# Kernel tuning notes

Measured on AMD Instinct MI355X. Metric: run time of the kernel, lower is better.

## Reference

```python
import jax, jax.numpy as jnp
import numpy as np

N_NODES = 100000
N_EDGES = 1500000
N_REL = 3
HID = 256


def setup_inputs() -> dict:
    key = jax.random.key(0)
    ks = jax.random.split(key, 8)
    return {
        "feat_a": jax.random.normal(ks[0], (N_NODES, 256), dtype=jnp.float32),
        "feat_b": jax.random.normal(ks[1], (N_NODES, 384), dtype=jnp.float32),
        "Wp_a": jax.random.normal(ks[2], (256, HID), dtype=jnp.float32) * 0.03,
        "Wp_b": jax.random.normal(ks[3], (384, HID), dtype=jnp.float32) * 0.03,
        "Wr": jax.random.normal(ks[4], (N_REL, HID, HID), dtype=jnp.float32) * 0.06,
        "ln_gamma": jnp.ones((HID,), dtype=jnp.float32),
        "ln_beta": jnp.zeros((HID,), dtype=jnp.float32),
        "edge_weight": jax.random.uniform(ks[5], (N_EDGES,), dtype=jnp.float32),
        "edge_src": jax.random.randint(ks[6], (N_EDGES,), 0, N_NODES, dtype=jnp.int32),
        "edge_dst": jax.random.randint(ks[7], (N_EDGES,), 0, N_NODES, dtype=jnp.int32),
    }


def _layer_norm(x, gamma, beta, eps=1e-5):
    mu = jnp.mean(x, axis=-1, keepdims=True)
    var = jnp.mean(jnp.square(x - mu), axis=-1, keepdims=True)
    return (x - mu) * jax.lax.rsqrt(var + eps) * gamma + beta


def reference(feat_a, feat_b, Wp_a, Wp_b, Wr, ln_gamma, ln_beta,
              edge_weight, edge_src, edge_dst):
    # avg fusion of modality projections (bias-free linears), padding node zeroed
    h0 = 0.5 * (feat_a @ Wp_a + feat_b @ Wp_b)  # [N, H]
    h0 = h0.at[0].set(0.0)

    n = h0.shape[0]
    e_per_rel = edge_src.shape[0] // N_REL  # edges pre-sorted by relation id
    aggregated = jnp.zeros_like(h0)
    for r in range(N_REL):
        s = slice(r * e_per_rel, (r + 1) * e_per_rel)
        src, dst, w = edge_src[s], edge_dst[s], edge_weight[s]
        # gather -> relation linear -> weight scale  [E_r, H]
        msg = (h0[src] @ Wr[r]) * w[:, None]
        num = jax.ops.segment_sum(msg, dst, num_segments=n)
        den = jax.ops.segment_sum(w, dst, num_segments=n)
        aggregated = aggregated + num / jnp.maximum(den, 1e-8)[:, None]

    # dropout p=0 / eval -> identity; residual + LayerNorm, padding node zeroed
    h1 = _layer_norm(h0 + aggregated, ln_gamma, ln_beta)
    h1 = h1.at[0].set(0.0)
    return h1
```

## Files before the change

### kernel.cpp

```cpp
#include <hip/hip_runtime.h>

#define N_NODES 100000
#define HID 256
#define N_EDGES 1500000
#define N_REL 3
#define E_PER_REL (N_EDGES / N_REL)
#define NKEYS (N_REL * N_NODES)
#define KP 640
#define KR 768

#define SCAN_CHUNK 1024
#define NSCANBLK ((NKEYS + SCAN_CHUNK - 1) / SCAN_CHUNK)

typedef __attribute__((ext_vector_type(8))) short bf16x8;
typedef __attribute__((ext_vector_type(4))) float f32x4;

__device__ __forceinline__ short f2bf(float x) {
    union { float f; unsigned u; } v; v.f = x;
    unsigned r = v.u + 0x7fffu + ((v.u >> 16) & 1u);
    return (short)(r >> 16);
}
__device__ __forceinline__ float bf2f(short h) {
    union { unsigned u; float f; } v;
    v.u = ((unsigned)(unsigned short)h) << 16;
    return v.f;
}
__device__ __forceinline__ int xorf(int r) { return (r & 3) ^ ((r >> 2) & 3); }

__device__ __forceinline__ void gload16(const void* g, void* l) {
    typedef const __attribute__((address_space(1))) unsigned int gq;
    typedef __attribute__((address_space(3))) unsigned int lq;
    __builtin_amdgcn_global_load_lds((gq*)g, (lq*)l, 16, 0, 0);
}

__global__ __launch_bounds__(256) void wprep_kernel(
    const float* __restrict__ Wa, const float* __restrict__ Wb,
    const float* __restrict__ Wr,
    short* __restrict__ WTp, short* __restrict__ WTr)
{
    int idx = blockIdx.x * 256 + threadIdx.x;
    if (idx < 256 * KP) {
        int c = idx / KP, k = idx - c * KP;
        float v = (k < 256) ? Wa[k * HID + c] : Wb[(k - 256) * HID + c];
        WTp[idx] = f2bf(0.5f * v);
    } else {
        int j = idx - 256 * KP;
        if (j < 256 * KR) {
            int c = j / KR, k = j - c * KR;
            WTr[j] = f2bf(Wr[(k >> 8) * HID * HID + (k & 255) * HID + c]);
        }
    }
}

__global__ __launch_bounds__(512, 4) void proj_gemm(
    const float* __restrict__ fa, const float* __restrict__ fb,
    const short* __restrict__ WTp, short* __restrict__ h0h)
{
    __shared__ float smA[2][128 * 32];
    __shared__ short smB[2][256 * 32];
    const int tid = threadIdx.x;
    const int lane = tid & 63;
    const int w = tid >> 6;
    const int wr = w >> 2, wc = w & 3;
    const int brow = blockIdx.x * 128;

    f32x4 acc[4][4] = {};

    const int a_r8 = lane >> 3;
    const int a_sl = (lane & 7) ^ a_r8;
    const int b_c16 = lane >> 2;

    int aRowG[2], bColL[2], bSl[2];
    #pragma unroll
    for (int ii = 0; ii < 2; ++ii) {
        int i = w * 2 + ii;
        int gr = brow + i * 8 + a_r8;
        aRowG[ii] = (gr < N_NODES) ? gr : (N_NODES - 1);
        bColL[ii] = i * 16 + b_c16;
        bSl[ii] = (lane & 3) ^ xorf(bColL[ii]);
    }

    auto stage = [&](int buf, int k0) {
        const float* asrc; int astr, kk;
        if (k0 < 256) { asrc = fa; astr = 256; kk = k0; }
        else          { asrc = fb; astr = 384; kk = k0 - 256; }
        #pragma unroll
        for (int ii = 0; ii < 2; ++ii) {
            int i = w * 2 + ii;
            gload16(asrc + (size_t)aRowG[ii] * astr + kk + a_sl * 4,
                    (char*)&smA[buf][0] + i * 1024);
        }
        #pragma unroll
        for (int ii = 0; ii < 2; ++ii) {
            int i = w * 2 + ii;
            gload16(WTp + (size_t)bColL[ii] * KP + k0 + bSl[ii] * 8,
                    (char*)&smB[buf][0] + i * 1024);
        }
    };

    stage(0, 0);
    __syncthreads();
    int cur = 0;
    for (int t = 0; t < KP / 32; ++t) {
        int knext = (t + 1) * 32;
        if (knext < KP) stage(cur ^ 1, knext);

        bf16x8 afr[4], bfr[4];
        #pragma unroll
        for (int m = 0; m < 4; ++m) {
            int rt = wr * 64 + m * 16 + (lane & 15);
            int p0 = (((lane >> 4) << 1) | 0) ^ (rt & 7);
            int p1 = (((lane >> 4) << 1) | 1) ^ (rt & 7);
            f32x4 lo = *(const f32x4*)((const char*)&smA[cur][0] + rt * 128 + p0 * 16);
            f32x4 hi = *(const f32x4*)((const char*)&smA[cur][0] + rt * 128 + p1 * 16);
            bf16x8 tb;
            tb[0] = f2bf(lo.x); tb[1] = f2bf(lo.y); tb[2] = f2bf(lo.z); tb[3] = f2bf(lo.w);
            tb[4] = f2bf(hi.x); tb[5] = f2bf(hi.y); tb[6] = f2bf(hi.z); tb[7] = f2bf(hi.w);
            afr[m] = tb;
        }
        #pragma unroll
        for (int n = 0; n < 4; ++n) {
            int ct = wc * 64 + n * 16 + (lane & 15);
            int p = (lane >> 4) ^ xorf(ct);
            bfr[n] = *(const bf16x8*)((const char*)&smB[cur][0] + ct * 64 + p * 16);
        }
        #pragma unroll
        for (int m = 0; m < 4; ++m)
            #pragma unroll
            for (int n = 0; n < 4; ++n)
                acc[m][n] = __builtin_amdgcn_mfma_f32_16x16x32_bf16(
                    afr[m], bfr[n], acc[m][n], 0, 0, 0);

        __syncthreads();
        cur ^= 1;
    }

    #pragma unroll
    for (int m = 0; m < 4; ++m) {
        #pragma unroll
        for (int j = 0; j < 4; ++j) {
            int row = brow + wr * 64 + m * 16 + ((lane >> 4) << 2) + j;
            if (row >= N_NODES) continue;
            #pragma unroll
            for (int n = 0; n < 4; ++n) {
                int col = wc * 64 + n * 16 + (lane & 15);
                short v = (row == 0) ? (short)0 : f2bf(acc[m][n][j]);
                h0h[(size_t)row * HID + col] = v;
            }
        }
    }
}

__global__ __launch_bounds__(512, 4) void rel_gemm_ln(
    const short* __restrict__ S, const short* __restrict__ WTr,
    const short* __restrict__ h0h,
    const float* __restrict__ gamma, const float* __restrict__ beta,
    float* __restrict__ out)
{
    __shared__ short smA[2][128 * 32];
    __shared__ short smB[2][256 * 32];
    __shared__ float redS[128][4];
    __shared__ float redS2[128][4];
    __shared__ float smMean[128], smRs[128];
    __shared__ float smG[256], smBt[256];
    const int tid = threadIdx.x;
    const int lane = tid & 63;
    const int w = tid >> 6;
    const int wr = w >> 2, wc = w & 3;
    const int brow = blockIdx.x * 128;

    if (tid < 256) { smG[tid] = gamma[tid]; smBt[tid] = beta[tid]; }

    f32x4 acc[4][4] = {};

    const int s_r16 = lane >> 2;
    const int sRowL = w * 16 + s_r16;
    int gr0 = brow + sRowL;
    const int sRowG = (gr0 < N_NODES) ? gr0 : (N_NODES - 1);
    const int sSl = (lane & 3) ^ xorf(sRowL);
    const int b_c16 = lane >> 2;
    int bColL[2], bSl[2];
    #pragma unroll
    for (int ii = 0; ii < 2; ++ii) {
        int i = w * 2 + ii;
        bColL[ii] = i * 16 + b_c16;
        bSl[ii] = (lane & 3) ^ xorf(bColL[ii]);
    }

    auto stage = [&](int buf, int k0) {
        gload16(S + (size_t)sRowG * KR + k0 + sSl * 8,
                (char*)&smA[buf][0] + w * 1024);
        #pragma unroll
        for (int ii = 0; ii < 2; ++ii) {
            int i = w * 2 + ii;
            gload16(WTr + (size_t)bColL[ii] * KR + k0 + bSl[ii] * 8,
                    (char*)&smB[buf][0] + i * 1024);
        }
    };

    stage(0, 0);
    __syncthreads();
    int cur = 0;
    for (int t = 0; t < KR / 32; ++t) {
        int knext = (t + 1) * 32;
        if (knext < KR) stage(cur ^ 1, knext);

        bf16x8 afr[4], bfr[4];
        #pragma unroll
        for (int m = 0; m < 4; ++m) {
            int rt = wr * 64 + m * 16 + (lane & 15);
            int p = (lane >> 4) ^ xorf(rt);
            afr[m] = *(const bf16x8*)((const char*)&smA[cur][0] + rt * 64 + p * 16);
        }
        #pragma unroll
        for (int n = 0; n < 4; ++n) {
            int ct = wc * 64 + n * 16 + (lane & 15);
            int p = (lane >> 4) ^ xorf(ct);
            bfr[n] = *(const bf16x8*)((const char*)&smB[cur][0] + ct * 64 + p * 16);
        }
        #pragma unroll
        for (int m = 0; m < 4; ++m)
            #pragma unroll
            for (int n = 0; n < 4; ++n)
                acc[m][n] = __builtin_amdgcn_mfma_f32_16x16x32_bf16(
                    afr[m], bfr[n], acc[m][n], 0, 0, 0);

        __syncthreads();
        cur ^= 1;
    }

    #pragma unroll
    for (int m = 0; m < 4; ++m) {
        #pragma unroll
        for (int j = 0; j < 4; ++j) {
            int lrow = wr * 64 + m * 16 + ((lane >> 4) << 2) + j;
            int grow = brow + lrow;
            int crow = (grow < N_NODES) ? grow : 0;
            float s = 0.f, s2 = 0.f;
            #pragma unroll
            for (int n = 0; n < 4; ++n) {
                int col = wc * 64 + n * 16 + (lane & 15);
                float x = acc[m][n][j] + bf2f(h0h[(size_t)crow * HID + col]);
                acc[m][n][j] = x;
                s += x; s2 = fmaf(x, x, s2);
            }
            #pragma unroll
            for (int off = 1; off < 16; off <<= 1) {
                s += __shfl_xor(s, off, 64);
                s2 += __shfl_xor(s2, off, 64);
            }
            if ((lane & 15) == 0) { redS[lrow][wc] = s; redS2[lrow][wc] = s2; }
        }
    }
    __syncthreads();
    if (tid < 128) {
        float tot  = redS[tid][0] + redS[tid][1] + redS[tid][2] + redS[tid][3];
        float tot2 = redS2[tid][0] + redS2[tid][1] + redS2[tid][2] + redS2[tid][3];
        float mean = tot * (1.0f / HID);
        float var = tot2 * (1.0f / HID) - mean * mean;
        smMean[tid] = mean;
        smRs[tid] = rsqrtf(var + 1e-5f);
    }
    __syncthreads();
    #pragma unroll
    for (int m = 0; m < 4; ++m) {
        #pragma unroll
        for (int j = 0; j < 4; ++j) {
            int lrow = wr * 64 + m * 16 + ((lane >> 4) << 2) + j;
            int grow = brow + lrow;
            if (grow >= N_NODES) continue;
            float mean = smMean[lrow], rs = smRs[lrow];
            #pragma unroll
            for (int n = 0; n < 4; ++n) {
                int col = wc * 64 + n * 16 + (lane & 15);
                float y = (acc[m][n][j] - mean) * rs * smG[col] + smBt[col];
                out[(size_t)grow * HID + col] = (grow == 0) ? 0.f : y;
            }
        }
    }
}

__global__ __launch_bounds__(256) void hist_kernel(
    const int* __restrict__ dst, int* __restrict__ count)
{
    int i = blockIdx.x * 256 + threadIdx.x;
    if (i >= N_EDGES) return;
    int r = i / E_PER_REL;
    atomicAdd(&count[r * N_NODES + dst[i]], 1);
}

__global__ __launch_bounds__(256) void scan1_kernel(
    const int* __restrict__ count, int* __restrict__ offset,
    int* __restrict__ bsum)
{
    __shared__ int tmp[256];
    const int t = threadIdx.x;
    const int base = blockIdx.x * SCAN_CHUNK + t * 4;
    int v[4];
    #pragma unroll
    for (int j = 0; j < 4; ++j)
        v[j] = (base + j < NKEYS) ? count[base + j] : 0;
    int tsum = v[0] + v[1] + v[2] + v[3];
    tmp[t] = tsum;
    __syncthreads();
    #pragma unroll
    for (int off = 1; off < 256; off <<= 1) {
        int x = (t >= off) ? tmp[t - off] : 0;
        __syncthreads();
        tmp[t] += x;
        __syncthreads();
    }
    int run = tmp[t] - tsum;
    #pragma unroll
    for (int j = 0; j < 4; ++j) {
        if (base + j < NKEYS) offset[base + j] = run;
        run += v[j];
    }
    if (t == 0) bsum[blockIdx.x] = tmp[255];
}

__global__ __launch_bounds__(256) void scan2_kernel(int* __restrict__ bsum)
{
    __shared__ int tmp[256];
    const int t = threadIdx.x;
    int v0 = (2 * t     < NSCANBLK) ? bsum[2 * t]     : 0;
    int v1 = (2 * t + 1 < NSCANBLK) ? bsum[2 * t + 1] : 0;
    int psum = v0 + v1;
    tmp[t] = psum;
    __syncthreads();
    #pragma unroll
    for (int off = 1; off < 256; off <<= 1) {
        int x = (t >= off) ? tmp[t - off] : 0;
        __syncthreads();
        tmp[t] += x;
        __syncthreads();
    }
    int excl = tmp[t] - psum;
    if (2 * t     < NSCANBLK) bsum[2 * t]     = excl;
    if (2 * t + 1 < NSCANBLK) bsum[2 * t + 1] = excl + v0;
}

__global__ __launch_bounds__(256) void scan3_kernel(
    int* __restrict__ offset, const int* __restrict__ bsum)
{
    int i = blockIdx.x * 256 + threadIdx.x;
    if (i >= NKEYS) return;
    offset[i] += bsum[i / SCAN_CHUNK];
}

__global__ __launch_bounds__(256) void fill_kernel(
    const int* __restrict__ src, const int* __restrict__ dst,
    const float* __restrict__ w,
    int* __restrict__ offset, int* __restrict__ csr_src,
    float* __restrict__ csr_w)
{
    int i = blockIdx.x * 256 + threadIdx.x;
    if (i >= N_EDGES) return;
    int r = i / E_PER_REL;
    int key = r * N_NODES + dst[i];
    int pos = atomicAdd(&offset[key], 1);
    csr_src[pos] = src[i];
    csr_w[pos] = w[i];
}

__global__ __launch_bounds__(256) void gather_kernel(
    const short* __restrict__ h0h,
    const int* __restrict__ ends, const int* __restrict__ count,
    const int* __restrict__ csr_src, const float* __restrict__ csr_w,
    short* __restrict__ S)
{
    int gw = (blockIdx.x * 256 + threadIdx.x) >> 6;
    int lane = threadIdx.x & 63;
    if (gw >= N_REL * N_NODES) return;
    int r = gw / N_NODES;
    int node = gw - r * N_NODES;
    int deg = count[gw];
    int end = ends[gw];
    int start = end - deg;
    const size_t colo = (size_t)lane * 4;

    float a0 = 0.f, a1 = 0.f, a2 = 0.f, a3 = 0.f;
    float den = 0.f;

    if (deg > 0) {
        int degc = (deg < 64) ? deg : 64;
        int myp = start + ((lane < degc) ? lane : 0);
        int msrc = csr_src[myp];
        float mw = (lane < degc) ? csr_w[myp] : 0.f;

        for (int p = 0; p < degc; p += 4) {
            #pragma unroll
            for (int j = 0; j < 4; ++j) {
                int q = p + j;
                bool ok = q < degc;
                int sj = __shfl(msrc, ok ? q : 0, 64);
                float wj = ok ? __shfl(mw, q, 64) : 0.f;
                short4 v = *(const short4*)(h0h + (size_t)sj * HID + colo);
                a0 = fmaf(wj, bf2f(v.x), a0);
                a1 = fmaf(wj, bf2f(v.y), a1);
                a2 = fmaf(wj, bf2f(v.z), a2);
                a3 = fmaf(wj, bf2f(v.w), a3);
                den += wj;
            }
        }
        for (int p = start + 64; p < end; ++p) {
            int s = csr_src[p];
            float wt = csr_w[p];
            short4 v = *(const short4*)(h0h + (size_t)s * HID + colo);
            a0 = fmaf(wt, bf2f(v.x), a0);
            a1 = fmaf(wt, bf2f(v.y), a1);
            a2 = fmaf(wt, bf2f(v.z), a2);
            a3 = fmaf(wt, bf2f(v.w), a3);
            den += wt;
        }
    }

    float inv = 1.0f / fmaxf(den, 1e-8f);
    short4 o;
    o.x = f2bf(a0 * inv);
    o.y = f2bf(a1 * inv);
    o.z = f2bf(a2 * inv);
    o.w = f2bf(a3 * inv);
    *(short4*)(S + (size_t)node * KR + r * HID + colo) = o;
}

extern "C" void kernel_launch(void* const* d_in, const int* in_sizes, int n_in,
                              void* d_out, int out_size, void* d_ws, size_t ws_size,
                              hipStream_t stream) {
    const float* fa    = (const float*)d_in[0];
    const float* fb    = (const float*)d_in[1];
    const float* Wa    = (const float*)d_in[2];
    const float* Wb    = (const float*)d_in[3];
    const float* Wr    = (const float*)d_in[4];
    const float* gamma = (const float*)d_in[5];
    const float* beta  = (const float*)d_in[6];
    const float* ew    = (const float*)d_in[7];
    const int*   esrc  = (const int*)d_in[8];
    const int*   edst  = (const int*)d_in[9];
    float* out = (float*)d_out;

    char* ws = (char*)d_ws;
    size_t off = 0;
    short* h0h     = (short*)(ws + off); off += (size_t)N_NODES * HID * 2;
    short* S       = (short*)(ws + off); off += (size_t)N_NODES * KR * 2;
    short* WTp     = (short*)(ws + off); off += (size_t)256 * KP * 2;
    short* WTr     = (short*)(ws + off); off += (size_t)256 * KR * 2;
    int*   count   = (int*)  (ws + off); off += (size_t)NKEYS * 4;
    int*   offs    = (int*)  (ws + off); off += (size_t)NKEYS * 4;
    int*   bsum    = (int*)  (ws + off); off += 4096;
    int*   csr_src = (int*)  (ws + off); off += (size_t)N_EDGES * 4;
    float* csr_w   = (float*)(ws + off); off += (size_t)N_EDGES * 4;

    wprep_kernel<<<(256 * KP + 256 * KR) / 256, 256, 0, stream>>>(
        Wa, Wb, Wr, WTp, WTr);

    const int ngrid = (N_NODES + 127) / 128;
    proj_gemm<<<ngrid, 512, 0, stream>>>(fa, fb, WTp, h0h);

    hipMemsetAsync(count, 0, (size_t)NKEYS * 4, stream);
    const int egrid = (N_EDGES + 255) / 256;
    hist_kernel<<<egrid, 256, 0, stream>>>(edst, count);
    scan1_kernel<<<NSCANBLK, 256, 0, stream>>>(count, offs, bsum);
    scan2_kernel<<<1, 256, 0, stream>>>(bsum);
    scan3_kernel<<<(NKEYS + 255) / 256, 256, 0, stream>>>(offs, bsum);
    fill_kernel<<<egrid, 256, 0, stream>>>(esrc, edst, ew, offs, csr_src, csr_w);

    gather_kernel<<<(N_REL * N_NODES * 64) / 256, 256, 0, stream>>>(
        h0h, offs, count, csr_src, csr_w, S);

    rel_gemm_ln<<<ngrid, 512, 0, stream>>>(S, WTr, h0h, gamma, beta, out);
}
```

Measured before the change: 527.7 us.

## Convert A tile to bf16 in registers before LDS and shrink shared memory

```diff
diff --git a/kernel.cpp b/kernel.cpp
--- a/kernel.cpp
+++ b/kernel.cpp
@@ -52,77 +52,71 @@
     }
 }
 
-__global__ __launch_bounds__(512, 4) void proj_gemm(
+__global__ __launch_bounds__(512, 8) void proj_gemm(
     const float* __restrict__ fa, const float* __restrict__ fb,
     const short* __restrict__ WTp, short* __restrict__ h0h)
 {
-    __shared__ float smA[2][128 * 32];
-    __shared__ short smB[2][256 * 32];
+    __shared__ alignas(16) char lds[49152];
     const int tid = threadIdx.x;
     const int lane = tid & 63;
     const int w = tid >> 6;
     const int wr = w >> 2, wc = w & 3;
     const int brow = blockIdx.x * 128;
 
+    auto smA = [&](int b) -> char* { return lds + b * 8192; };
+    auto smB = [&](int b) -> char* { return lds + 16384 + b * 16384; };
+
     f32x4 acc[4][4] = {};
 
-    const int a_r8 = lane >> 3;
-    const int a_sl = (lane & 7) ^ a_r8;
+    const int arow = tid >> 2;
+    const int akq = tid & 3;
+    int gr = brow + arow;
+    const int garow = (gr < N_NODES) ? gr : (N_NODES - 1);
+    const int aslot = akq ^ xorf(arow);
     const int b_c16 = lane >> 2;
-
-    int aRowG[2], bColL[2], bSl[2];
+    int bColL[2], bSl[2];
     #pragma unroll
     for (int ii = 0; ii < 2; ++ii) {
         int i = w * 2 + ii;
-        int gr = brow + i * 8 + a_r8;
-        aRowG[ii] = (gr < N_NODES) ? gr : (N_NODES - 1);
         bColL[ii] = i * 16 + b_c16;
         bSl[ii] = (lane & 3) ^ xorf(bColL[ii]);
     }
 
-    auto stage = [&](int buf, int k0) {
+    auto loadA = [&](int k0, f32x4& o0, f32x4& o1) {
         const float* asrc; int astr, kk;
         if (k0 < 256) { asrc = fa; astr = 256; kk = k0; }
         else          { asrc = fb; astr = 384; kk = k0 - 256; }
-        #pragma unroll
-        for (int ii = 0; ii < 2; ++ii) {
-            int i = w * 2 + ii;
-            gload16(asrc + (size_t)aRowG[ii] * astr + kk + a_sl * 4,
-                    (char*)&smA[buf][0] + i * 1024);
-        }
+        const float* ap = asrc + (size_t)garow * astr + kk + akq * 8;
+        o0 = *(const f32x4*)(ap + 0);
+        o1 = *(const f32x4*)(ap + 4);
+    };
+    auto writeA = [&](int buf, const f32x4& v0, const f32x4& v1) {
+        bf16x8 ha;
+        ha[0] = f2bf(v0.x); ha[1] = f2bf(v0.y); ha[2] = f2bf(v0.z); ha[3] = f2bf(v0.w);
+        ha[4] = f2bf(v1.x); ha[5] = f2bf(v1.y); ha[6] = f2bf(v1.z); ha[7] = f2bf(v1.w);
+        *(bf16x8*)(smA(buf) + arow * 64 + aslot * 16) = ha;
+    };
+    auto stageB = [&](int buf, int k0) {
         #pragma unroll
         for (int ii = 0; ii < 2; ++ii) {
             int i = w * 2 + ii;
             gload16(WTp + (size_t)bColL[ii] * KP + k0 + bSl[ii] * 8,
-                    (char*)&smB[buf][0] + i * 1024);
+                    smB(buf) + i * 1024);
         }
     };
-
-    stage(0, 0);
-    __syncthreads();
-    int cur = 0;
-    for (int t = 0; t < KP / 32; ++t) {
-        int knext = (t + 1) * 32;
-        if (knext < KP) stage(cur ^ 1, knext);
-
+    auto compute = [&](int buf) {
         bf16x8 afr[4], bfr[4];
         #pragma unroll
         for (int m = 0; m < 4; ++m) {
             int rt = wr * 64 + m * 16 + (lane & 15);
-            int p0 = (((lane >> 4) << 1) | 0) ^ (rt & 7);
-            int p1 = (((lane >> 4) << 1) | 1) ^ (rt & 7);
-            f32x4 lo = *(const f32x4*)((const char*)&smA[cur][0] + rt * 128 + p0 * 16);
-            f32x4 hi = *(const f32x4*)((const char*)&smA[cur][0] + rt * 128 + p1 * 16);
-            bf16x8 tb;
-            tb[0] = f2bf(lo.x); tb[1] = f2bf(lo.y); tb[2] = f2bf(lo.z); tb[3] = f2bf(lo.w);
-            tb[4] = f2bf(hi.x); tb[5] = f2bf(hi.y); tb[6] = f2bf(hi.z); tb[7] = f2bf(hi.w);
-            afr[m] = tb;
+            int p = (lane >> 4) ^ xorf(rt);
+            afr[m] = *(const bf16x8*)(smA(buf) + rt * 64 + p * 16);
         }
         #pragma unroll
         for (int n = 0; n < 4; ++n) {
             int ct = wc * 64 + n * 16 + (lane & 15);
             int p = (lane >> 4) ^ xorf(ct);
-            bfr[n] = *(const bf16x8*)((const char*)&smB[cur][0] + ct * 64 + p * 16);
+            bfr[n] = *(const bf16x8*)(smB(buf) + ct * 64 + p * 16);
         }
         #pragma unroll
         for (int m = 0; m < 4; ++m)
@@ -130,9 +124,29 @@
             for (int n = 0; n < 4; ++n)
                 acc[m][n] = __builtin_amdgcn_mfma_f32_16x16x32_bf16(
                     afr[m], bfr[n], acc[m][n], 0, 0, 0);
-
-        __syncthreads();
-        cur ^= 1;
+    };
+
+    const int nt = KP / 32;
+    f32x4 p0, p1, q0, q1;
+    loadA(0, p0, p1);
+    stageB(0, 0);
+    loadA(32, q0, q1);
+    writeA(0, p0, p1);
+    __syncthreads();
+
+    for (int t = 0; t < nt; t += 2) {
+        writeA(1, q0, q1);
+        stageB(1, (t + 1) * 32);
+        if (t + 2 < nt) loadA((t + 2) * 32, p0, p1);
+        compute(0);
+        __syncthreads();
+        if (t + 2 < nt) {
+            writeA(0, p0, p1);
+            stageB(0, (t + 2) * 32);
+            if (t + 3 < nt) loadA((t + 3) * 32, q0, q1);
+        }
+        compute(1);
+        __syncthreads();
     }
 
     #pragma unroll
@@ -151,25 +165,21 @@
     }
 }
 
-__global__ __launch_bounds__(512, 4) void rel_gemm_ln(
+__global__ __launch_bounds__(512, 8) void rel_gemm_ln(
     const short* __restrict__ S, const short* __restrict__ WTr,
     const short* __restrict__ h0h,
     const float* __restrict__ gamma, const float* __restrict__ beta,
     float* __restrict__ out)
 {
-    __shared__ short smA[2][128 * 32];
-    __shared__ short smB[2][256 * 32];
-    __shared__ float redS[128][4];
-    __shared__ float redS2[128][4];
-    __shared__ float smMean[128], smRs[128];
-    __shared__ float smG[256], smBt[256];
+    __shared__ alignas(16) char lds[49152];
     const int tid = threadIdx.x;
     const int lane = tid & 63;
     const int w = tid >> 6;
     const int wr = w >> 2, wc = w & 3;
     const int brow = blockIdx.x * 128;
 
-    if (tid < 256) { smG[tid] = gamma[tid]; smBt[tid] = beta[tid]; }
+    auto smA = [&](int b) -> char* { return lds + b * 8192; };
+    auto smB = [&](int b) -> char* { return lds + 16384 + b * 16384; };
 
     f32x4 acc[4][4] = {};
 
@@ -188,13 +198,12 @@
     }
 
     auto stage = [&](int buf, int k0) {
-        gload16(S + (size_t)sRowG * KR + k0 + sSl * 8,
-                (char*)&smA[buf][0] + w * 1024);
+        gload16(S + (size_t)sRowG * KR + k0 + sSl * 8, smA(buf) + w * 1024);
         #pragma unroll
         for (int ii = 0; ii < 2; ++ii) {
             int i = w * 2 + ii;
             gload16(WTr + (size_t)bColL[ii] * KR + k0 + bSl[ii] * 8,
-                    (char*)&smB[buf][0] + i * 1024);
+                    smB(buf) + i * 1024);
         }
     };
 
@@ -210,13 +219,13 @@
         for (int m = 0; m < 4; ++m) {
             int rt = wr * 64 + m * 16 + (lane & 15);
             int p = (lane >> 4) ^ xorf(rt);
-            afr[m] = *(const bf16x8*)((const char*)&smA[cur][0] + rt * 64 + p * 16);
+            afr[m] = *(const bf16x8*)(smA(cur) + rt * 64 + p * 16);
         }
         #pragma unroll
         for (int n = 0; n < 4; ++n) {
             int ct = wc * 64 + n * 16 + (lane & 15);
             int p = (lane >> 4) ^ xorf(ct);
-            bfr[n] = *(const bf16x8*)((const char*)&smB[cur][0] + ct * 64 + p * 16);
+            bfr[n] = *(const bf16x8*)(smB(cur) + ct * 64 + p * 16);
         }
         #pragma unroll
         for (int m = 0; m < 4; ++m)
@@ -227,6 +236,19 @@
 
         __syncthreads();
         cur ^= 1;
+    }
+
+    float* redS  = (float*)lds;
+    float* redS2 = redS + 512;
+    float* smMean = redS2 + 512;
+    float* smRs   = smMean + 128;
+
+    float gk[4], bk[4];
+    #pragma unroll
+    for (int n = 0; n < 4; ++n) {
+        int col = wc * 64 + n * 16 + (lane & 15);
+        gk[n] = gamma[col];
+        bk[n] = beta[col];
     }
 
     #pragma unroll
@@ -249,13 +271,13 @@
                 s += __shfl_xor(s, off, 64);
                 s2 += __shfl_xor(s2, off, 64);
             }
-            if ((lane & 15) == 0) { redS[lrow][wc] = s; redS2[lrow][wc] = s2; }
+            if ((lane & 15) == 0) { redS[lrow * 4 + wc] = s; redS2[lrow * 4 + wc] = s2; }
         }
     }
     __syncthreads();
     if (tid < 128) {
-        float tot  = redS[tid][0] + redS[tid][1] + redS[tid][2] + redS[tid][3];
-        float tot2 = redS2[tid][0] + redS2[tid][1] + redS2[tid][2] + redS2[tid][3];
+        float tot  = redS[tid * 4 + 0] + redS[tid * 4 + 1] + redS[tid * 4 + 2] + redS[tid * 4 + 3];
+        float tot2 = redS2[tid * 4 + 0] + redS2[tid * 4 + 1] + redS2[tid * 4 + 2] + redS2[tid * 4 + 3];
         float mean = tot * (1.0f / HID);
         float var = tot2 * (1.0f / HID) - mean * mean;
         smMean[tid] = mean;
@@ -273,7 +295,7 @@
             #pragma unroll
             for (int n = 0; n < 4; ++n) {
                 int col = wc * 64 + n * 16 + (lane & 15);
-                float y = (acc[m][n][j] - mean) * rs * smG[col] + smBt[col];
+                float y = (acc[m][n][j] - mean) * rs * gk[n] + bk[n];
                 out[(size_t)grow * HID + col] = (grow == 0) ? 0.f : y;
             }
         }
```

Measured after the change: 521.2 us. About the same (-1.2%).

## Triple-buffer LDS staging in both GEMMs with explicit vmcnt waits

Applied to the files above, without the earlier changes.

```diff
diff --git a/kernel.cpp b/kernel.cpp
--- a/kernel.cpp
+++ b/kernel.cpp
@@ -52,35 +52,41 @@
     }
 }
 
-__global__ __launch_bounds__(512, 4) void proj_gemm(
+__global__ __launch_bounds__(512, 2) void proj_gemm(
     const float* __restrict__ fa, const float* __restrict__ fb,
     const short* __restrict__ WTp, short* __restrict__ h0h)
 {
-    __shared__ float smA[2][128 * 32];
-    __shared__ short smB[2][256 * 32];
+    __shared__ alignas(16) char lds[98304];
     const int tid = threadIdx.x;
     const int lane = tid & 63;
     const int w = tid >> 6;
     const int wr = w >> 2, wc = w & 3;
     const int brow = blockIdx.x * 128;
 
+    auto bufA = [&](int b) -> char* { return lds + b * 32768; };
+    auto bufB = [&](int b) -> char* { return lds + b * 32768 + 16384; };
+
     f32x4 acc[4][4] = {};
 
     const int a_r8 = lane >> 3;
     const int a_sl = (lane & 7) ^ a_r8;
-    const int b_c16 = lane >> 2;
-
-    int aRowG[2], bColL[2], bSl[2];
+    int aRowG[2];
     #pragma unroll
     for (int ii = 0; ii < 2; ++ii) {
         int i = w * 2 + ii;
         int gr = brow + i * 8 + a_r8;
         aRowG[ii] = (gr < N_NODES) ? gr : (N_NODES - 1);
+    }
+    const int b_c16 = lane >> 2;
+    int bColL[2], bSl[2];
+    #pragma unroll
+    for (int ii = 0; ii < 2; ++ii) {
+        int i = w * 2 + ii;
         bColL[ii] = i * 16 + b_c16;
         bSl[ii] = (lane & 3) ^ xorf(bColL[ii]);
     }
 
-    auto stage = [&](int buf, int k0) {
+    auto stage = [&](int b, int k0) {
         const float* asrc; int astr, kk;
         if (k0 < 256) { asrc = fa; astr = 256; kk = k0; }
         else          { asrc = fb; astr = 384; kk = k0 - 256; }
@@ -88,22 +94,24 @@
         for (int ii = 0; ii < 2; ++ii) {
             int i = w * 2 + ii;
             gload16(asrc + (size_t)aRowG[ii] * astr + kk + a_sl * 4,
-                    (char*)&smA[buf][0] + i * 1024);
+                    bufA(b) + i * 1024);
         }
         #pragma unroll
         for (int ii = 0; ii < 2; ++ii) {
             int i = w * 2 + ii;
             gload16(WTp + (size_t)bColL[ii] * KP + k0 + bSl[ii] * 8,
-                    (char*)&smB[buf][0] + i * 1024);
+                    bufB(b) + i * 1024);
         }
     };
 
-    stage(0, 0);
-    __syncthreads();
+    const int nt = KP / 32;
+    stage(0, 0); stage(1, 32); stage(2, 64);
     int cur = 0;
-    for (int t = 0; t < KP / 32; ++t) {
-        int knext = (t + 1) * 32;
-        if (knext < KP) stage(cur ^ 1, knext);
+    for (int t = 0; t < nt; ++t) {
+        if (t < nt - 2)       asm volatile("s_waitcnt vmcnt(8)" ::: "memory");
+        else if (t == nt - 2) asm volatile("s_waitcnt vmcnt(4)" ::: "memory");
+        else                  asm volatile("s_waitcnt vmcnt(0)" ::: "memory");
+        __builtin_amdgcn_s_barrier();
 
         bf16x8 afr[4], bfr[4];
         #pragma unroll
@@ -111,8 +119,8 @@
             int rt = wr * 64 + m * 16 + (lane & 15);
             int p0 = (((lane >> 4) << 1) | 0) ^ (rt & 7);
             int p1 = (((lane >> 4) << 1) | 1) ^ (rt & 7);
-            f32x4 lo = *(const f32x4*)((const char*)&smA[cur][0] + rt * 128 + p0 * 16);
-            f32x4 hi = *(const f32x4*)((const char*)&smA[cur][0] + rt * 128 + p1 * 16);
+            f32x4 lo = *(const f32x4*)(bufA(cur) + rt * 128 + p0 * 16);
+            f32x4 hi = *(const f32x4*)(bufA(cur) + rt * 128 + p1 * 16);
             bf16x8 tb;
             tb[0] = f2bf(lo.x); tb[1] = f2bf(lo.y); tb[2] = f2bf(lo.z); tb[3] = f2bf(lo.w);
             tb[4] = f2bf(hi.x); tb[5] = f2bf(hi.y); tb[6] = f2bf(hi.z); tb[7] = f2bf(hi.w);
@@ -122,7 +130,7 @@
         for (int n = 0; n < 4; ++n) {
             int ct = wc * 64 + n * 16 + (lane & 15);
             int p = (lane >> 4) ^ xorf(ct);
-            bfr[n] = *(const bf16x8*)((const char*)&smB[cur][0] + ct * 64 + p * 16);
+            bfr[n] = *(const bf16x8*)(bufB(cur) + ct * 64 + p * 16);
         }
         #pragma unroll
         for (int m = 0; m < 4; ++m)
@@ -131,8 +139,11 @@
                 acc[m][n] = __builtin_amdgcn_mfma_f32_16x16x32_bf16(
                     afr[m], bfr[n], acc[m][n], 0, 0, 0);
 
-        __syncthreads();
-        cur ^= 1;
+        asm volatile("s_waitcnt lgkmcnt(0)" ::: "memory");
+        __builtin_amdgcn_sched_barrier(0);
+        __builtin_amdgcn_s_barrier();
+        if (t + 3 < nt) stage(cur, (t + 3) * 32);
+        cur = (cur == 2) ? 0 : cur + 1;
     }
 
     #pragma unroll
@@ -157,19 +168,15 @@
     const float* __restrict__ gamma, const float* __restrict__ beta,
     float* __restrict__ out)
 {
-    __shared__ short smA[2][128 * 32];
-    __shared__ short smB[2][256 * 32];
-    __shared__ float redS[128][4];
-    __shared__ float redS2[128][4];
-    __shared__ float smMean[128], smRs[128];
-    __shared__ float smG[256], smBt[256];
+    __shared__ alignas(16) char lds[73728];
     const int tid = threadIdx.x;
     const int lane = tid & 63;
     const int w = tid >> 6;
     const int wr = w >> 2, wc = w & 3;
     const int brow = blockIdx.x * 128;
 
-    if (tid < 256) { smG[tid] = gamma[tid]; smBt[tid] = beta[tid]; }
+    auto bufA = [&](int b) -> char* { return lds + b * 24576; };
+    auto bufB = [&](int b) -> char* { return lds + b * 24576 + 8192; };
 
     f32x4 acc[4][4] = {};
 
@@ -187,36 +194,37 @@
         bSl[ii] = (lane & 3) ^ xorf(bColL[ii]);
     }
 
-    auto stage = [&](int buf, int k0) {
-        gload16(S + (size_t)sRowG * KR + k0 + sSl * 8,
-                (char*)&smA[buf][0] + w * 1024);
+    auto stage = [&](int b, int k0) {
+        gload16(S + (size_t)sRowG * KR + k0 + sSl * 8, bufA(b) + w * 1024);
         #pragma unroll
         for (int ii = 0; ii < 2; ++ii) {
             int i = w * 2 + ii;
             gload16(WTr + (size_t)bColL[ii] * KR + k0 + bSl[ii] * 8,
-                    (char*)&smB[buf][0] + i * 1024);
+                    bufB(b) + i * 1024);
         }
     };
 
-    stage(0, 0);
-    __syncthreads();
+    const int nt = KR / 32;
+    stage(0, 0); stage(1, 32); stage(2, 64);
     int cur = 0;
-    for (int t = 0; t < KR / 32; ++t) {
-        int knext = (t + 1) * 32;
-        if (knext < KR) stage(cur ^ 1, knext);
+    for (int t = 0; t < nt; ++t) {
+        if (t < nt - 2)       asm volatile("s_waitcnt vmcnt(6)" ::: "memory");
+        else if (t == nt - 2) asm volatile("s_waitcnt vmcnt(3)" ::: "memory");
+        else                  asm volatile("s_waitcnt vmcnt(0)" ::: "memory");
+        __builtin_amdgcn_s_barrier();
 
         bf16x8 afr[4], bfr[4];
         #pragma unroll
         for (int m = 0; m < 4; ++m) {
             int rt = wr * 64 + m * 16 + (lane & 15);
             int p = (lane >> 4) ^ xorf(rt);
-            afr[m] = *(const bf16x8*)((const char*)&smA[cur][0] + rt * 64 + p * 16);
+            afr[m] = *(const bf16x8*)(bufA(cur) + rt * 64 + p * 16);
         }
         #pragma unroll
         for (int n = 0; n < 4; ++n) {
             int ct = wc * 64 + n * 16 + (lane & 15);
             int p = (lane >> 4) ^ xorf(ct);
-            bfr[n] = *(const bf16x8*)((const char*)&smB[cur][0] + ct * 64 + p * 16);
+            bfr[n] = *(const bf16x8*)(bufB(cur) + ct * 64 + p * 16);
         }
         #pragma unroll
         for (int m = 0; m < 4; ++m)
@@ -225,8 +233,24 @@
                 acc[m][n] = __builtin_amdgcn_mfma_f32_16x16x32_bf16(
                     afr[m], bfr[n], acc[m][n], 0, 0, 0);
 
-        __syncthreads();
-        cur ^= 1;
+        asm volatile("s_waitcnt lgkmcnt(0)" ::: "memory");
+        __builtin_amdgcn_sched_barrier(0);
+        __builtin_amdgcn_s_barrier();
+        if (t + 3 < nt) stage(cur, (t + 3) * 32);
+        cur = (cur == 2) ? 0 : cur + 1;
+    }
+
+    float* redS  = (float*)lds;
+    float* redS2 = redS + 512;
+    float* smMean = redS2 + 512;
+    float* smRs   = smMean + 128;
+
+    float gk[4], bk[4];
+    #pragma unroll
+    for (int n = 0; n < 4; ++n) {
+        int col = wc * 64 + n * 16 + (lane & 15);
+        gk[n] = gamma[col];
+        bk[n] = beta[col];
     }
 
     #pragma unroll
@@ -249,13 +273,13 @@
                 s += __shfl_xor(s, off, 64);
                 s2 += __shfl_xor(s2, off, 64);
             }
-            if ((lane & 15) == 0) { redS[lrow][wc] = s; redS2[lrow][wc] = s2; }
+            if ((lane & 15) == 0) { redS[lrow * 4 + wc] = s; redS2[lrow * 4 + wc] = s2; }
         }
     }
     __syncthreads();
     if (tid < 128) {
-        float tot  = redS[tid][0] + redS[tid][1] + redS[tid][2] + redS[tid][3];
-        float tot2 = redS2[tid][0] + redS2[tid][1] + redS2[tid][2] + redS2[tid][3];
+        float tot  = redS[tid * 4 + 0] + redS[tid * 4 + 1] + redS[tid * 4 + 2] + redS[tid * 4 + 3];
+        float tot2 = redS2[tid * 4 + 0] + redS2[tid * 4 + 1] + redS2[tid * 4 + 2] + redS2[tid * 4 + 3];
         float mean = tot * (1.0f / HID);
         float var = tot2 * (1.0f / HID) - mean * mean;
         smMean[tid] = mean;
@@ -273,7 +297,7 @@
             #pragma unroll
             for (int n = 0; n < 4; ++n) {
                 int col = wc * 64 + n * 16 + (lane & 15);
-                float y = (acc[m][n][j] - mean) * rs * smG[col] + smBt[col];
+                float y = (acc[m][n][j] - mean) * rs * gk[n] + bk[n];
                 out[(size_t)grow * HID + col] = (grow == 0) ? 0.f : y;
             }
         }
```

Measured after the change: 501.9 us. 4.9% less time.
